# Optimization experiments

Hardware: AMD Instinct MI355X
Metric: run time of the kernel (lower is better)

Reference implementation:

```python
import jax, jax.numpy as jnp
import numpy as np

N_MOL = 128      # molecules per batch (per side)
ATOMS = 32       # atoms per molecule
N_AT = N_MOL * ATOMS
DIM = 64
NFP = 10000
LAYER_HIDDEN = 3
LAYER_OUTPUT = 2
DESC = 55
FEAT = 2 * DIM + 59  # 187


def _block_diag_adj(k, seg):
    # random dense adjacency masked to the block-diagonal structure produced by pad()
    a = jax.random.uniform(k, (N_AT, N_AT), dtype=jnp.float32)
    mask = (seg[:, None] == seg[None, :]).astype(jnp.float32)
    return a * mask


def setup_inputs() -> dict:
    key = jax.random.key(0)
    ks = jax.random.split(key, 24)
    seg = jnp.repeat(jnp.arange(N_MOL), ATOMS)  # molecule id per atom (sorted)
    inp = {
        'adj_D': _block_diag_adj(ks[0], seg),
        'adj_A': _block_diag_adj(ks[1], seg),
        'fp_D': jax.random.randint(ks[2], (N_AT,), 0, NFP),
        'fp_A': jax.random.randint(ks[3], (N_AT,), 0, NFP),
        'seg_D': seg,
        'seg_A': seg,
        'homo_D': jax.random.normal(ks[4], (N_MOL, 1), dtype=jnp.float32),
        'lumo_D': jax.random.normal(ks[5], (N_MOL, 1), dtype=jnp.float32),
        'homo_A': jax.random.normal(ks[6], (N_MOL, 1), dtype=jnp.float32),
        'lumo_A': jax.random.normal(ks[7], (N_MOL, 1), dtype=jnp.float32),
        'descriptors': jax.random.normal(ks[8], (N_MOL, DESC), dtype=jnp.float32),
        'correct_values': jax.random.normal(ks[9], (N_MOL, 1), dtype=jnp.float32),
        'embed': jax.random.normal(ks[10], (NFP, DIM), dtype=jnp.float32),
        'Wf_w': jax.random.normal(ks[11], (LAYER_HIDDEN, DIM, DIM), dtype=jnp.float32) * (1.0 / np.sqrt(DIM)),
        'Wf_b': jax.random.normal(ks[12], (LAYER_HIDDEN, DIM), dtype=jnp.float32) * 0.01,
        'Wo_w': jax.random.normal(ks[13], (LAYER_OUTPUT, FEAT, FEAT), dtype=jnp.float32) * (1.0 / np.sqrt(FEAT)),
        'Wo_b': jax.random.normal(ks[14], (LAYER_OUTPUT, FEAT), dtype=jnp.float32) * 0.01,
        'Wp_w': jax.random.normal(ks[15], (1, FEAT), dtype=jnp.float32) * (1.0 / np.sqrt(FEAT)),
        'Wp_b': jax.random.normal(ks[16], (1,), dtype=jnp.float32) * 0.01,
    }
    return inp


def _l2norm(h):
    # torch F.normalize(h, 2, 1): x / max(||x||_2, eps)
    n = jnp.sqrt(jnp.sum(h * h, axis=1, keepdims=True))
    return h / jnp.maximum(n, 1e-12)


def _gnn_side(adj, v, Wf_w, Wf_b):
    for l in range(LAYER_HIDDEN):
        h = jax.nn.relu(v @ Wf_w[l].T + Wf_b[l])  # [N_AT, DIM]
        v = _l2norm(h + adj @ h)                   # residual + block-diag message passing
    return v


def reference(adj_D, adj_A, fp_D, fp_A, seg_D, seg_A,
              homo_D, lumo_D, homo_A, lumo_A, descriptors, correct_values,
              embed, Wf_w, Wf_b, Wo_w, Wo_b, Wp_w, Wp_b):
    v_D = embed[fp_D]
    v_A = embed[fp_A]
    v_D = _gnn_side(adj_D, v_D, Wf_w, Wf_b)
    v_A = _gnn_side(adj_A, v_A, Wf_w, Wf_b)
    mol_D = jax.ops.segment_sum(v_D, seg_D, num_segments=N_MOL)  # sum-pool per molecule
    mol_A = jax.ops.segment_sum(v_A, seg_A, num_segments=N_MOL)
    x = jnp.concatenate([mol_D, homo_D, lumo_D, mol_A, homo_A, lumo_A, descriptors], axis=1)  # [N_MOL, 187]
    for l in range(LAYER_OUTPUT):
        x = jax.nn.relu(x @ Wo_w[l].T + Wo_b[l])
    pred = x @ Wp_w.T + Wp_b  # [N_MOL, 1]
    loss = jnp.mean((pred - correct_values) ** 2)
    return loss
```

## Files before the change

kernel.cpp:

```cpp
#include <hip/hip_runtime.h>

#define N_MOL 128
#define ATOMS 32
#define N_AT  4096
#define DIM   64
#define FEAT  187
#define PADV  68
#define PADA  33

__global__ __launch_bounds__(512) void gnn_kernel(
    const float* __restrict__ adj_D, const float* __restrict__ adj_A,
    const int*   __restrict__ fp_D,  const int*   __restrict__ fp_A,
    const float* __restrict__ embed,
    const float* __restrict__ Wf_w,  const float* __restrict__ Wf_b,
    float* __restrict__ mol_out )
{
    __shared__ float wT_s[3][DIM][DIM];
    __shared__ float b_s[3][DIM];
    __shared__ float v_s[ATOMS][PADV];
    __shared__ float h_s[ATOMS][PADV];
    __shared__ float adj_s[ATOMS][PADA];

    const int blk  = blockIdx.x;
    const int side = blk >> 7;
    const int m    = blk & 127;
    const float* adj = side ? adj_A : adj_D;
    const int*   fp  = side ? fp_A  : fp_D;
    const int tid = threadIdx.x;

    for (int i4 = tid; i4 < 3 * DIM * DIM / 4; i4 += 512) {
        float4 w = ((const float4*)Wf_w)[i4];
        int i  = i4 << 2;
        int l  = i >> 12;
        int d  = (i >> 6) & 63;
        int k0 = i & 63;
        const float* wp = (const float*)&w;
        #pragma unroll
        for (int kk = 0; kk < 4; ++kk) {
            int k  = k0 + kk;
            int dg = (d >> 2) ^ (k & 15);
            wT_s[l][k][(dg << 2) + (d & 3)] = wp[kk];
        }
    }
    if (tid < 3 * DIM) ((float*)b_s)[tid] = Wf_b[tid];

    for (int i4 = tid; i4 < ATOMS * ATOMS / 4; i4 += 512) {
        int r  = i4 >> 3;
        int c4 = (i4 & 7) << 2;
        float4 av = *(const float4*)&adj[(size_t)(m * ATOMS + r) * N_AT + m * ATOMS + c4];
        adj_s[r][c4 + 0] = av.x; adj_s[r][c4 + 1] = av.y;
        adj_s[r][c4 + 2] = av.z; adj_s[r][c4 + 3] = av.w;
    }
    {
        int a  = tid >> 4;
        int d4 = (tid & 15) << 2;
        float4 ev = *(const float4*)&embed[(size_t)fp[m * ATOMS + a] * DIM + d4];
        *(float4*)&v_s[a][d4] = ev;
    }
    __syncthreads();

    const int a  = tid >> 4;
    const int g  = tid & 15;
    const int d0 = g << 2;

    for (int l = 0; l < 3; ++l) {
        float accv[4];
        *(float4*)accv = *(const float4*)&b_s[l][d0];
        const float* vrow = v_s[a];
        #pragma unroll
        for (int k0 = 0; k0 < DIM; k0 += 4) {
            float4 vv = *(const float4*)&vrow[k0];
            const float* vp = (const float*)&vv;
            #pragma unroll
            for (int kk = 0; kk < 4; ++kk) {
                int k = k0 + kk;
                float4 ww = *(const float4*)&wT_s[l][k][(g ^ (k & 15)) << 2];
                float vs = vp[kk];
                accv[0] += vs * ww.x; accv[1] += vs * ww.y;
                accv[2] += vs * ww.z; accv[3] += vs * ww.w;
            }
        }
        float4 hst;
        hst.x = fmaxf(accv[0], 0.0f); hst.y = fmaxf(accv[1], 0.0f);
        hst.z = fmaxf(accv[2], 0.0f); hst.w = fmaxf(accv[3], 0.0f);
        *(float4*)&h_s[a][d0] = hst;
        __syncthreads();

        float4 tv = *(const float4*)&h_s[a][d0];
        float t0 = tv.x, t1 = tv.y, t2 = tv.z, t3 = tv.w;
        const float* arow = adj_s[a];
        #pragma unroll 8
        for (int b = 0; b < ATOMS; ++b) {
            float ab = arow[b];
            float4 hb = *(const float4*)&h_s[b][d0];
            t0 += ab * hb.x; t1 += ab * hb.y; t2 += ab * hb.z; t3 += ab * hb.w;
        }
        float ss = t0 * t0 + t1 * t1 + t2 * t2 + t3 * t3;
        #pragma unroll
        for (int msk = 1; msk < 16; msk <<= 1)
            ss += __shfl_xor(ss, msk);
        float scale = 1.0f / fmaxf(sqrtf(ss), 1e-12f);
        float4 sv; sv.x = t0 * scale; sv.y = t1 * scale; sv.z = t2 * scale; sv.w = t3 * scale;
        *(float4*)&v_s[a][d0] = sv;
        __syncthreads();
    }

    if (tid < DIM) {
        float s = 0.0f;
        #pragma unroll 8
        for (int aa = 0; aa < ATOMS; ++aa) s += v_s[aa][tid];
        mol_out[(size_t)side * N_MOL * DIM + m * DIM + tid] = s;
    }
}

__global__ __launch_bounds__(256) void head_kernel(
    const float* __restrict__ mol,
    const float* __restrict__ homo_D, const float* __restrict__ lumo_D,
    const float* __restrict__ homo_A, const float* __restrict__ lumo_A,
    const float* __restrict__ desc,   const float* __restrict__ cv,
    const float* __restrict__ Wo_w,   const float* __restrict__ Wo_b,
    const float* __restrict__ Wp_w,   const float* __restrict__ Wp_b,
    float* __restrict__ sq_out )
{
    __shared__ float x_s[FEAT + 1];
    __shared__ float y_s[FEAT + 1];
    __shared__ float red_s[256];

    const int m = blockIdx.x;
    const int t = threadIdx.x;

    if (t < 64) x_s[t] = mol[m * DIM + t];
    if (t >= 64 && t < 128) x_s[66 + (t - 64)] = mol[N_MOL * DIM + m * DIM + (t - 64)];
    if (t >= 128 && t < 183) x_s[132 + (t - 128)] = desc[m * 55 + (t - 128)];
    if (t == 183) x_s[64]  = homo_D[m];
    if (t == 184) x_s[65]  = lumo_D[m];
    if (t == 185) x_s[130] = homo_A[m];
    if (t == 186) x_s[131] = lumo_A[m];
    __syncthreads();

    float* xin  = x_s;
    float* xout = y_s;
    for (int l = 0; l < 2; ++l) {
        float acc = 0.0f;
        if (t < FEAT) {
            acc = Wo_b[l * FEAT + t];
            const float* wr = Wo_w + ((size_t)l * FEAT + t) * FEAT;
            int k = 0;
            #pragma unroll 1
            for (; k < 184; k += 4) {
                acc += xin[k] * wr[k] + xin[k+1] * wr[k+1]
                     + xin[k+2] * wr[k+2] + xin[k+3] * wr[k+3];
            }
            acc += xin[184] * wr[184] + xin[185] * wr[185] + xin[186] * wr[186];
            acc = fmaxf(acc, 0.0f);
        }
        __syncthreads();
        if (t < FEAT) xout[t] = acc;
        __syncthreads();
        float* tmp = xin; xin = xout; xout = tmp;
    }

    red_s[t] = (t < FEAT) ? xin[t] * Wp_w[t] : 0.0f;
    __syncthreads();
    for (int s = 128; s > 0; s >>= 1) {
        if (t < s) red_s[t] += red_s[t + s];
        __syncthreads();
    }
    if (t == 0) {
        float pred = red_s[0] + Wp_b[0];
        float d = pred - cv[m];
        sq_out[m] = d * d;
    }
}

__global__ __launch_bounds__(64) void loss_kernel(
    const float* __restrict__ sq, float* __restrict__ out)
{
    const int t = threadIdx.x;
    float v = sq[t] + sq[t + 64];
    #pragma unroll
    for (int msk = 32; msk >= 1; msk >>= 1)
        v += __shfl_xor(v, msk);
    if (t == 0) out[0] = v * (1.0f / 128.0f);
}

extern "C" void kernel_launch(void* const* d_in, const int* in_sizes, int n_in,
                              void* d_out, int out_size, void* d_ws, size_t ws_size,
                              hipStream_t stream) {
    const float* adj_D  = (const float*)d_in[0];
    const float* adj_A  = (const float*)d_in[1];
    const int*   fp_D   = (const int*)  d_in[2];
    const int*   fp_A   = (const int*)  d_in[3];
    const float* homo_D = (const float*)d_in[6];
    const float* lumo_D = (const float*)d_in[7];
    const float* homo_A = (const float*)d_in[8];
    const float* lumo_A = (const float*)d_in[9];
    const float* desc   = (const float*)d_in[10];
    const float* cv     = (const float*)d_in[11];
    const float* embed  = (const float*)d_in[12];
    const float* Wf_w   = (const float*)d_in[13];
    const float* Wf_b   = (const float*)d_in[14];
    const float* Wo_w   = (const float*)d_in[15];
    const float* Wo_b   = (const float*)d_in[16];
    const float* Wp_w   = (const float*)d_in[17];
    const float* Wp_b   = (const float*)d_in[18];

    float* ws  = (float*)d_ws;
    float* mol = ws;
    float* sq  = ws + 2 * N_MOL * DIM;

    gnn_kernel<<<256, 512, 0, stream>>>(adj_D, adj_A, fp_D, fp_A, embed,
                                        Wf_w, Wf_b, mol);
    head_kernel<<<N_MOL, 256, 0, stream>>>(mol, homo_D, lumo_D, homo_A, lumo_A,
                                           desc, cv, Wo_w, Wo_b, Wp_w, Wp_b, sq);
    loss_kernel<<<1, 64, 0, stream>>>(sq, (float*)d_out);
}
```

Measured before the change: 200.2 us.

## Restructure MLP head into transposed per-layer kernels with feature-major activations

The GNN kernel now writes pooled molecule vectors and scalar descriptors directly into a feature-major transposed activation buffer. The old per-molecule head kernel, where each block read all of Wo from global memory, is replaced by one kernel per output layer: each block handles one output feature, and threads run over molecules, so weight reads are broadcast and activation reads coalesce. The prediction and loss are fused into a single kernel. This adds one more launch and a grid-wide dependency between layers, but removes the redundant weight streaming across 128 blocks.

```diff
diff --git a/kernel.cpp b/kernel.cpp
--- a/kernel.cpp
+++ b/kernel.cpp
@@ -13,7 +13,10 @@
     const int*   __restrict__ fp_D,  const int*   __restrict__ fp_A,
     const float* __restrict__ embed,
     const float* __restrict__ Wf_w,  const float* __restrict__ Wf_b,
-    float* __restrict__ mol_out )
+    const float* __restrict__ homo_D, const float* __restrict__ lumo_D,
+    const float* __restrict__ homo_A, const float* __restrict__ lumo_A,
+    const float* __restrict__ desc,
+    float* __restrict__ xT )
 {
     __shared__ float wT_s[3][DIM][DIM];
     __shared__ float b_s[3][DIM];
@@ -109,79 +112,80 @@
         float s = 0.0f;
         #pragma unroll 8
         for (int aa = 0; aa < ATOMS; ++aa) s += v_s[aa][tid];
-        mol_out[(size_t)side * N_MOL * DIM + m * DIM + tid] = s;
-    }
-}
-
-__global__ __launch_bounds__(256) void head_kernel(
-    const float* __restrict__ mol,
-    const float* __restrict__ homo_D, const float* __restrict__ lumo_D,
-    const float* __restrict__ homo_A, const float* __restrict__ lumo_A,
-    const float* __restrict__ desc,   const float* __restrict__ cv,
-    const float* __restrict__ Wo_w,   const float* __restrict__ Wo_b,
-    const float* __restrict__ Wp_w,   const float* __restrict__ Wp_b,
-    float* __restrict__ sq_out )
+        xT[(side * 66 + tid) * N_MOL + m] = s;
+    }
+    if (side == 0) {
+        if (tid == 64) xT[64 * N_MOL + m]  = homo_D[m];
+        if (tid == 65) xT[65 * N_MOL + m]  = lumo_D[m];
+        if (tid == 66) xT[130 * N_MOL + m] = homo_A[m];
+        if (tid == 67) xT[131 * N_MOL + m] = lumo_A[m];
+        if (tid >= 68 && tid < 68 + 55)
+            xT[(132 + tid - 68) * N_MOL + m] = desc[m * 55 + (tid - 68)];
+    }
+}
+
+__global__ __launch_bounds__(128) void head_layer_kernel(
+    const float* __restrict__ xT_in,
+    float* __restrict__ xT_out,
+    const float* __restrict__ W,
+    const float* __restrict__ b)
 {
-    __shared__ float x_s[FEAT + 1];
-    __shared__ float y_s[FEAT + 1];
-    __shared__ float red_s[256];
-
-    const int m = blockIdx.x;
-    const int t = threadIdx.x;
-
-    if (t < 64) x_s[t] = mol[m * DIM + t];
-    if (t >= 64 && t < 128) x_s[66 + (t - 64)] = mol[N_MOL * DIM + m * DIM + (t - 64)];
-    if (t >= 128 && t < 183) x_s[132 + (t - 128)] = desc[m * 55 + (t - 128)];
-    if (t == 183) x_s[64]  = homo_D[m];
-    if (t == 184) x_s[65]  = lumo_D[m];
-    if (t == 185) x_s[130] = homo_A[m];
-    if (t == 186) x_s[131] = lumo_A[m];
-    __syncthreads();
-
-    float* xin  = x_s;
-    float* xout = y_s;
-    for (int l = 0; l < 2; ++l) {
-        float acc = 0.0f;
-        if (t < FEAT) {
-            acc = Wo_b[l * FEAT + t];
-            const float* wr = Wo_w + ((size_t)l * FEAT + t) * FEAT;
-            int k = 0;
-            #pragma unroll 1
-            for (; k < 184; k += 4) {
-                acc += xin[k] * wr[k] + xin[k+1] * wr[k+1]
-                     + xin[k+2] * wr[k+2] + xin[k+3] * wr[k+3];
-            }
-            acc += xin[184] * wr[184] + xin[185] * wr[185] + xin[186] * wr[186];
-            acc = fmaxf(acc, 0.0f);
-        }
-        __syncthreads();
-        if (t < FEAT) xout[t] = acc;
-        __syncthreads();
-        float* tmp = xin; xin = xout; xout = tmp;
-    }
-
-    red_s[t] = (t < FEAT) ? xin[t] * Wp_w[t] : 0.0f;
-    __syncthreads();
-    for (int s = 128; s > 0; s >>= 1) {
-        if (t < s) red_s[t] += red_s[t + s];
-        __syncthreads();
-    }
-    if (t == 0) {
-        float pred = red_s[0] + Wp_b[0];
-        float d = pred - cv[m];
-        sq_out[m] = d * d;
-    }
-}
-
-__global__ __launch_bounds__(64) void loss_kernel(
-    const float* __restrict__ sq, float* __restrict__ out)
+    const int f = blockIdx.x;
+    const int m = threadIdx.x;
+    const float* wr = W + (size_t)f * FEAT;
+
+    float acc = b[f];
+    int k = 0;
+    #pragma unroll 2
+    for (; k + 8 <= FEAT; k += 8) {
+        float acc0 = wr[k+0] * xT_in[(k+0) * N_MOL + m]
+                   + wr[k+1] * xT_in[(k+1) * N_MOL + m]
+                   + wr[k+2] * xT_in[(k+2) * N_MOL + m]
+                   + wr[k+3] * xT_in[(k+3) * N_MOL + m];
+        float acc1 = wr[k+4] * xT_in[(k+4) * N_MOL + m]
+                   + wr[k+5] * xT_in[(k+5) * N_MOL + m]
+                   + wr[k+6] * xT_in[(k+6) * N_MOL + m]
+                   + wr[k+7] * xT_in[(k+7) * N_MOL + m];
+        acc += acc0 + acc1;
+    }
+    for (; k < FEAT; ++k) acc += wr[k] * xT_in[k * N_MOL + m];
+
+    xT_out[(size_t)f * N_MOL + m] = fmaxf(acc, 0.0f);
+}
+
+__global__ __launch_bounds__(128) void predloss_kernel(
+    const float* __restrict__ xT,
+    const float* __restrict__ Wp_w, const float* __restrict__ Wp_b,
+    const float* __restrict__ cv,
+    float* __restrict__ out)
 {
-    const int t = threadIdx.x;
-    float v = sq[t] + sq[t + 64];
+    __shared__ float p_s[2];
+    const int m = threadIdx.x;
+
+    float acc = Wp_b[0];
+    int f = 0;
+    #pragma unroll 2
+    for (; f + 8 <= FEAT; f += 8) {
+        float a0 = Wp_w[f+0] * xT[(f+0) * N_MOL + m]
+                 + Wp_w[f+1] * xT[(f+1) * N_MOL + m]
+                 + Wp_w[f+2] * xT[(f+2) * N_MOL + m]
+                 + Wp_w[f+3] * xT[(f+3) * N_MOL + m];
+        float a1 = Wp_w[f+4] * xT[(f+4) * N_MOL + m]
+                 + Wp_w[f+5] * xT[(f+5) * N_MOL + m]
+                 + Wp_w[f+6] * xT[(f+6) * N_MOL + m]
+                 + Wp_w[f+7] * xT[(f+7) * N_MOL + m];
+        acc += a0 + a1;
+    }
+    for (; f < FEAT; ++f) acc += Wp_w[f] * xT[f * N_MOL + m];
+
+    float d = acc - cv[m];
+    float v = d * d;
     #pragma unroll
     for (int msk = 32; msk >= 1; msk >>= 1)
         v += __shfl_xor(v, msk);
-    if (t == 0) out[0] = v * (1.0f / 128.0f);
+    if ((m & 63) == 0) p_s[m >> 6] = v;
+    __syncthreads();
+    if (m == 0) out[0] = (p_s[0] + p_s[1]) * (1.0f / 128.0f);
 }
 
 extern "C" void kernel_launch(void* const* d_in, const int* in_sizes, int n_in,
@@ -206,12 +210,16 @@
     const float* Wp_b   = (const float*)d_in[18];
 
     float* ws  = (float*)d_ws;
-    float* mol = ws;
-    float* sq  = ws + 2 * N_MOL * DIM;
+    float* xT0 = ws;
+    float* xT1 = ws + FEAT * N_MOL;
 
     gnn_kernel<<<256, 512, 0, stream>>>(adj_D, adj_A, fp_D, fp_A, embed,
-                                        Wf_w, Wf_b, mol);
-    head_kernel<<<N_MOL, 256, 0, stream>>>(mol, homo_D, lumo_D, homo_A, lumo_A,
-                                           desc, cv, Wo_w, Wo_b, Wp_w, Wp_b, sq);
-    loss_kernel<<<1, 64, 0, stream>>>(sq, (float*)d_out);
-}
+                                        Wf_w, Wf_b,
+                                        homo_D, lumo_D, homo_A, lumo_A, desc,
+                                        xT0);
+    head_layer_kernel<<<FEAT, 128, 0, stream>>>(xT0, xT1, Wo_w, Wo_b);
+    head_layer_kernel<<<FEAT, 128, 0, stream>>>(xT1, xT0,
+                                                Wo_w + (size_t)FEAT * FEAT,
+                                                Wo_b + FEAT);
+    predloss_kernel<<<1, 128, 0, stream>>>(xT0, Wp_w, Wp_b, cv, (float*)d_out);
+}
```

New measurement: 195.2 us. 1.03x faster.
